# Kernel optimization log

Hardware: AMD Instinct MI355X
Metric: run time of the kernel (lower is better)

Reference implementation:

```python
import jax, jax.numpy as jnp
import numpy as np

B, S, D = 4, 2048, 1024
H, DH = 16, 64
SCALE = DH ** -0.5


def setup_inputs() -> dict:
    key = jax.random.key(0)
    ks = jax.random.split(key, 7)
    x_q = jax.random.normal(ks[0], (B, S, D), dtype=jnp.float32)
    x_k = jax.random.normal(ks[1], (B, S, D), dtype=jnp.float32)
    x_v = jax.random.normal(ks[2], (B, S, D), dtype=jnp.float32)
    # causal mask: True means masked (matches torch masked_fill semantics)
    mask = jnp.triu(jnp.ones((S, S), dtype=bool), k=1)
    # Linear init: randn(in, out) / sqrt(out), no bias
    Wq = jax.random.normal(ks[3], (D, H * DH), dtype=jnp.float32) / np.sqrt(H * DH)
    Wk = jax.random.normal(ks[4], (D, H * DH), dtype=jnp.float32) / np.sqrt(H * DH)
    Wv = jax.random.normal(ks[5], (D, H * DH), dtype=jnp.float32) / np.sqrt(H * DH)
    Wo = jax.random.normal(ks[6], (H * DH, D), dtype=jnp.float32) / np.sqrt(D)
    return {"x_q": x_q, "x_k": x_k, "x_v": x_v, "mask": mask,
            "Wq": Wq, "Wk": Wk, "Wv": Wv, "Wo": Wo}


def reference(x_q, x_k, x_v, mask, Wq, Wk, Wv, Wo):
    def split_heads(x):  # [B,S,H*DH] -> [B,H,S,DH]
        return x.reshape(B, S, H, DH).transpose(0, 2, 1, 3)

    q = split_heads(x_q @ Wq)
    k = split_heads(x_k @ Wk)
    v = split_heads(x_v @ Wv)
    attn = jnp.einsum('bhqd,bhkd->bhqk', q, k) * SCALE
    attn = jnp.where(mask, -jnp.inf, attn)
    w_attn = jax.nn.softmax(attn, axis=-1)  # dropout p=0.0 is identity
    out = jnp.einsum('bhqk,bhkd->bhqd', w_attn, v)
    out = out.transpose(0, 2, 1, 3).reshape(B, S, H * DH)
    return out @ Wo
```

## Files before the change

kernel.cpp:

```cpp
#include <hip/hip_runtime.h>
#include <hip/hip_bf16.h>
#include <math.h>

#define BB 4
#define SS 2048
#define DD 1024
#define HH 16
#define DHE 64
#define NH (HH*DHE)
constexpr float NEG_BIG = -1e30f;

typedef __bf16 bf16x8 __attribute__((ext_vector_type(8)));
typedef float  f32x4  __attribute__((ext_vector_type(4)));

#define WAITVM6()   asm volatile("s_waitcnt vmcnt(6)" ::: "memory")
#define WAITVM4()   asm volatile("s_waitcnt vmcnt(4)" ::: "memory")
#define WAITVM0()   asm volatile("s_waitcnt vmcnt(0)" ::: "memory")
#define WAITLGKM0() asm volatile("s_waitcnt lgkmcnt(0)" ::: "memory")
#define MEMFENCE()  asm volatile("" ::: "memory")

__device__ __forceinline__ void gl_lds16(const __bf16* g, __bf16* l) {
  __builtin_amdgcn_global_load_lds(
      (const __attribute__((address_space(1))) unsigned int*)g,
      (__attribute__((address_space(3))) unsigned int*)l, 16, 0, 0);
}

__device__ __forceinline__ unsigned pack_bf2(float lo, float hi) {
  union { __bf16 h[2]; unsigned u; } p;
  p.h[0] = (__bf16)lo; p.h[1] = (__bf16)hi;
  return p.u;
}

__global__ __launch_bounds__(256) void cvt_k(
    const float* __restrict__ x0, const float* __restrict__ x1,
    const float* __restrict__ x2,
    __bf16* __restrict__ o0, __bf16* __restrict__ o1, __bf16* __restrict__ o2) {
  const float* x = blockIdx.z == 0 ? x0 : blockIdx.z == 1 ? x1 : x2;
  __bf16*      o = blockIdx.z == 0 ? o0 : blockIdx.z == 1 ? o1 : o2;
  const size_t n8 = (size_t)BB * SS * DD / 8;
  for (size_t i = (size_t)blockIdx.x * 256 + threadIdx.x; i < n8;
       i += (size_t)gridDim.x * 256) {
    f32x4 a = *(const f32x4*)(x + i * 8);
    f32x4 b = *(const f32x4*)(x + i * 8 + 4);
    bf16x8 v;
    #pragma unroll
    for (int j = 0; j < 4; j++) { v[j] = (__bf16)a[j]; v[j + 4] = (__bf16)b[j]; }
    *(bf16x8*)(o + i * 8) = v;
  }
}

__global__ __launch_bounds__(256) void wtrans_k(
    const float* __restrict__ w0, const float* __restrict__ w1,
    const float* __restrict__ w2, const float* __restrict__ w3,
    __bf16* __restrict__ o0, __bf16* __restrict__ o1,
    __bf16* __restrict__ o2, __bf16* __restrict__ o3) {
  __shared__ __bf16 t[32][33];
  const float* w = blockIdx.z == 0 ? w0 : blockIdx.z == 1 ? w1 : blockIdx.z == 2 ? w2 : w3;
  __bf16*      o = blockIdx.z == 0 ? o0 : blockIdx.z == 1 ? o1 : blockIdx.z == 2 ? o2 : o3;
  int tx = threadIdx.x & 31, ty = threadIdx.x >> 5;
  int bk = blockIdx.x * 32, bn = blockIdx.y * 32;
  #pragma unroll
  for (int i = 0; i < 4; i++)
    t[ty + i * 8][tx] = (__bf16)w[(size_t)(bk + ty + i * 8) * DD + bn + tx];
  __syncthreads();
  #pragma unroll
  for (int i = 0; i < 4; i++)
    o[(size_t)(bn + ty + i * 8) * DD + bk + tx] = t[tx][ty + i * 8];
}

__global__ __launch_bounds__(256) void vtrans_k(
    const __bf16* __restrict__ v, __bf16* __restrict__ o) {
  __shared__ __bf16 t[32][33];
  int tx = threadIdx.x & 31, ty = threadIdx.x >> 5;
  int bs = blockIdx.x * 32, bc = blockIdx.y * 32;
  const __bf16* vz = v + (size_t)blockIdx.z * SS * NH;
  __bf16*       oz = o + (size_t)blockIdx.z * NH * SS;
  #pragma unroll
  for (int i = 0; i < 4; i++)
    t[ty + i * 8][tx] = vz[(size_t)(bs + ty + i * 8) * NH + bc + tx];
  __syncthreads();
  #pragma unroll
  for (int i = 0; i < 4; i++)
    oz[(size_t)(bc + ty + i * 8) * SS + bs + tx] = t[tx][ty + i * 8];
}

struct B3 {
  const void*  a0; const void*  a1; const void*  a2;
  const __bf16* b0; const __bf16* b1; const __bf16* b2;
  void* c0; void* c1; void* c2;
};

template <typename CT>
__global__ __launch_bounds__(256, 3) void gemm_bb(B3 p) {
  __shared__ __bf16 Asr[3][128][32];
  __shared__ __bf16 Bsr[3][128][32];

  const unsigned nwg  = gridDim.x * gridDim.y * gridDim.z;
  const unsigned flat = blockIdx.x + gridDim.x * (blockIdx.y + gridDim.y * blockIdx.z);
  const unsigned swz  = (flat & 7) * (nwg >> 3) + (flat >> 3);
  const int bx = swz % gridDim.x;
  const unsigned rem = swz / gridDim.x;
  const int by = rem % gridDim.y;
  const int z  = rem / gridDim.y;

  const __bf16* __restrict__ A  = (const __bf16*)(z == 0 ? p.a0 : z == 1 ? p.a1 : p.a2);
  const __bf16* __restrict__ BT = z == 0 ? p.b0 : z == 1 ? p.b1 : p.b2;
  CT* __restrict__ C = (CT*)(z == 0 ? p.c0 : z == 1 ? p.c1 : p.c2);

  const int tid  = threadIdx.x;
  const int wave = tid >> 6, lane = tid & 63;
  const int quad = lane >> 4, l16 = lane & 15;
  const int wr = (wave >> 1) * 64, wc = (wave & 1) * 64;
  const int m0 = by * 128, n0 = bx * 128;

  f32x4 acc[4][4] = {};

  auto issue = [&](int it, int slot) {
    const int k0 = it * 32;
    const int rr  = lane >> 2;
    const int seg = (lane & 3) ^ ((rr >> 1) & 3);
    #pragma unroll
    for (int i = 0; i < 2; i++) {
      const int row = wave * 16 + i * 64 + rr;
      gl_lds16(&A [(size_t)(m0 + row) * DD + k0 + seg * 8], &Asr[slot][wave * 16 + i * 64][0]);
      gl_lds16(&BT[(size_t)(n0 + row) * DD + k0 + seg * 8], &Bsr[slot][wave * 16 + i * 64][0]);
    }
  };

  auto compute = [&](int s) {
    bf16x8 af[4], bfr[4];
    const int ph = (quad ^ ((l16 >> 1) & 3)) * 8;
    #pragma unroll
    for (int t = 0; t < 4; t++) {
      af[t]  = *(const bf16x8*)&Asr[s][wr + t * 16 + l16][ph];
      bfr[t] = *(const bf16x8*)&Bsr[s][wc + t * 16 + l16][ph];
    }
    __builtin_amdgcn_s_setprio(1);
    #pragma unroll
    for (int mt = 0; mt < 4; mt++)
      #pragma unroll
      for (int nt = 0; nt < 4; nt++)
        acc[mt][nt] = __builtin_amdgcn_mfma_f32_16x16x32_bf16(af[mt], bfr[nt], acc[mt][nt], 0, 0, 0);
    __builtin_amdgcn_s_setprio(0);
  };

  issue(0, 0); MEMFENCE();
  issue(1, 1); MEMFENCE();

  int cur = 0, pre = 2;
  #pragma unroll 1
  for (int it = 0; it < 30; it++) {
    WAITVM4();
    __builtin_amdgcn_s_barrier();
    issue(it + 2, pre);
    compute(cur);
    cur = cur == 2 ? 0 : cur + 1;
    pre = pre == 2 ? 0 : pre + 1;
  }
  WAITVM4(); __builtin_amdgcn_s_barrier(); compute(cur);
  cur = cur == 2 ? 0 : cur + 1;
  WAITVM0(); __builtin_amdgcn_s_barrier(); compute(cur);

  #pragma unroll
  for (int mt = 0; mt < 4; mt++)
    #pragma unroll
    for (int nt = 0; nt < 4; nt++)
      #pragma unroll
      for (int r = 0; r < 4; r++) {
        int row = m0 + wr + mt * 16 + quad * 4 + r;
        int col = n0 + wc + nt * 16 + l16;
        C[(size_t)row * NH + col] = (CT)acc[mt][nt][r];
      }
}

template <typename AT> struct AStage;
template <> struct AStage<float>  { f32x4 d[2][2]; };
template <> struct AStage<__bf16> { bf16x8 d[2]; };

template <typename AT, typename CT>
__global__ __launch_bounds__(256, 3) void gemm_bt(B3 p, size_t aoff) {
  __shared__ __bf16 As[128][40];
  __shared__ __bf16 Bs[4][128][32];
  const unsigned nwg  = gridDim.x * gridDim.y * gridDim.z;
  const unsigned flat = blockIdx.x + gridDim.x * (blockIdx.y + gridDim.y * blockIdx.z);
  const unsigned swz  = (flat & 7) * (nwg >> 3) + (flat >> 3);
  const int bx = swz % gridDim.x;
  const unsigned rem = swz / gridDim.x;
  const int by = rem % gridDim.y;
  const int z  = rem / gridDim.y;

  const AT* __restrict__ A = (const AT*)(z == 0 ? p.a0 : z == 1 ? p.a1 : p.a2);
  const __bf16* __restrict__ BT = z == 0 ? p.b0 : z == 1 ? p.b1 : p.b2;
  CT* __restrict__ C = (CT*)(z == 0 ? p.c0 : z == 1 ? p.c1 : p.c2);

  const int tid  = threadIdx.x;
  const int wave = tid >> 6, lane = tid & 63;
  const int quad = lane >> 4, l16 = lane & 15;
  const int wr = (wave >> 1) * 64, wc = (wave & 1) * 64;
  const int m0 = by * 128, n0 = bx * 128;

  f32x4 acc[4][4] = {};
  AStage<AT> aA, aB;

  auto loadA = [&](int k0, AStage<AT>& S) {
    #pragma unroll
    for (int i = 0; i < 2; i++) {
      int c = tid + i * 256;
      int row = c >> 2, seg = (c & 3) * 8;
      if constexpr (sizeof(AT) == 4) {
        const float* ap = (const float*)A + aoff + (size_t)(m0 + row) * DD + k0 + seg;
        S.d[i][0] = *(const f32x4*)ap;
        S.d[i][1] = *(const f32x4*)(ap + 4);
      } else {
        S.d[i] = *(const bf16x8*)((const __bf16*)A + aoff + (size_t)(m0 + row) * DD + k0 + seg);
      }
    }
  };
  auto issueB = [&](int k0, int buf) {
    #pragma unroll
    for (int i = 0; i < 2; i++) {
      int rr  = lane >> 2;
      int row = wave * 16 + i * 64 + rr;
      int seg = (lane & 3) ^ ((rr >> 1) & 3);
      gl_lds16(&BT[(size_t)(n0 + row) * DD + k0 + seg * 8],
               &Bs[buf][wave * 16 + i * 64][0]);
    }
  };

  auto step = [&](int it, AStage<AT>& S, bool last, bool tail) {
    if (last) { WAITVM0(); }
    else if constexpr (sizeof(AT) == 4) { WAITVM6(); }
    else { WAITVM4(); }
    __builtin_amdgcn_s_barrier();
    #pragma unroll
    for (int i = 0; i < 2; i++) {
      int c = tid + i * 256;
      bf16x8 av;
      if constexpr (sizeof(AT) == 4) {
        #pragma unroll
        for (int j = 0; j < 4; j++) {
          av[j]     = (__bf16)S.d[i][0][j];
          av[j + 4] = (__bf16)S.d[i][1][j];
        }
      } else {
        av = S.d[i];
      }
      *(bf16x8*)&As[c >> 2][(c & 3) * 8] = av;
    }
    WAITLGKM0();
    __builtin_amdgcn_s_barrier();
    if (!tail) {
      issueB((it + 2) * 32, (it + 2) & 3);
      loadA((it + 2) * 32, S);
    }
    const int buf = it & 3;
    bf16x8 af[4], bfr[4];
    #pragma unroll
    for (int t = 0; t < 4; t++) {
      af[t]  = *(const bf16x8*)&As[wr + t * 16 + l16][quad * 8];
      bfr[t] = *(const bf16x8*)&Bs[buf][wc + t * 16 + l16][(quad ^ ((l16 >> 1) & 3)) * 8];
    }
    __builtin_amdgcn_s_setprio(1);
    #pragma unroll
    for (int mt = 0; mt < 4; mt++)
      #pragma unroll
      for (int nt = 0; nt < 4; nt++)
        acc[mt][nt] = __builtin_amdgcn_mfma_f32_16x16x32_bf16(af[mt], bfr[nt], acc[mt][nt], 0, 0, 0);
    __builtin_amdgcn_s_setprio(0);
  };

  issueB(0, 0);  loadA(0, aA);
  MEMFENCE();
  issueB(32, 1); loadA(32, aB);
  MEMFENCE();

  for (int it2 = 0; it2 < 15; it2++) {
    step(2 * it2,     aA, false, false);
    step(2 * it2 + 1, aB, false, false);
  }
  step(30, aA, false, true);
  step(31, aB, true,  true);

  #pragma unroll
  for (int mt = 0; mt < 4; mt++)
    #pragma unroll
    for (int nt = 0; nt < 4; nt++)
      #pragma unroll
      for (int r = 0; r < 4; r++) {
        int row = m0 + wr + mt * 16 + quad * 4 + r;
        int col = n0 + wc + nt * 16 + l16;
        C[(size_t)row * NH + col] = (CT)acc[mt][nt][r];
      }
}

__global__ __launch_bounds__(256, 4) void attn_k(
    const __bf16* __restrict__ Q, const __bf16* __restrict__ K,
    const __bf16* __restrict__ VT, __bf16* __restrict__ O) {
  __shared__ __bf16 Ks[64][68];
  __shared__ __bf16 Vs[64][68];

  const int tid  = threadIdx.x;
  const int wave = tid >> 6, lane = tid & 63;
  const int quad = lane >> 4, l16 = lane & 15;

  const int n    = blockIdx.x;
  const int xcd  = n & 7, slot = n >> 3;
  const int gidx = xcd + 8 * (slot >> 4);
  const int bx   = slot & 15;
  const int h = gidx & 15, z = gidx >> 4;

  const __bf16* Qg = Q + (size_t)z * SS * NH + h * DHE;
  const __bf16* Kg = K + (size_t)z * SS * NH + h * DHE;
  const __bf16* Vg = VT + ((size_t)z * HH + h) * DHE * SS;
  __bf16*       Og = O + (size_t)z * SS * NH + h * DHE;

  bf16x8 kreg[2], vreg[2];
  auto loadKV = [&](int k0) {
    #pragma unroll
    for (int i = 0; i < 2; i++) {
      int v = tid + i * 256;
      kreg[i] = *(const bf16x8*)&Kg[(size_t)(k0 + (v >> 3)) * NH + (v & 7) * 8];
      vreg[i] = *(const bf16x8*)&Vg[(size_t)(v >> 3) * SS + k0 + (v & 7) * 8];
    }
  };

  #pragma unroll 1
  for (int seg = 0; seg < 2; seg++) {
    const int qt = seg ? bx : 31 - bx;
    const int q0 = qt * 64;
    const int ntiles = qt + 1;

    const int qrow = q0 + wave * 16 + l16;
    bf16x8 qf[2];
    #pragma unroll
    for (int kk = 0; kk < 2; kk++) {
      bf16x8 t = *(const bf16x8*)&Qg[(size_t)qrow * NH + kk * 32 + quad * 8];
      #pragma unroll
      for (int j = 0; j < 8; j++) t[j] = (__bf16)((float)t[j] * 0.125f);
      qf[kk] = t;
    }

    loadKV(0);
    float prows = 0.f;
    f32x4 oacc[4] = {};

    for (int kt = 0; kt < ntiles; kt++) {
      const int k0 = kt * 64;
      __syncthreads();
      #pragma unroll
      for (int i = 0; i < 2; i++) {
        int v = tid + i * 256;
        *(bf16x8*)&Ks[v >> 3][(v & 7) * 8] = kreg[i];
        *(bf16x8*)&Vs[v >> 3][(v & 7) * 8] = vreg[i];
      }
      __syncthreads();
      if (kt + 1 < ntiles) loadKV(k0 + 64);

      const bool diag = (kt == ntiles - 1);
      const int nq  = diag ? wave + 1 : 4;
      const int nsm = diag ? ((wave + 2) & ~1) : 4;
      const int nkk = nsm >> 1;

      f32x4 sc[4] = {};
      __builtin_amdgcn_s_setprio(1);
      #pragma unroll
      for (int kk = 0; kk < 2; kk++)
        #pragma unroll
        for (int nt = 0; nt < 4; nt++)
          if (nt < nq) {
            bf16x8 kf = *(const bf16x8*)&Ks[nt * 16 + l16][kk * 32 + quad * 8];
            sc[nt] = __builtin_amdgcn_mfma_f32_16x16x32_bf16(kf, qf[kk], sc[nt], 0, 0, 0);
          }
      __builtin_amdgcn_s_setprio(0);

      bf16x8 pf[2];
      #pragma unroll
      for (int t = 0; t < 2; t++)
        if (t < nkk) {
          const int nt0 = 2 * t, nt1 = 2 * t + 1;
          float pA[4], pB[4];
          #pragma unroll
          for (int r = 0; r < 4; r++) {
            float v0 = sc[nt0][r], v1 = sc[nt1][r];
            if (diag) {
              const int kb = k0 + quad * 4 + r;
              if (kb + nt0 * 16 > qrow) v0 = NEG_BIG;
              if (kb + nt1 * 16 > qrow) v1 = NEG_BIG;
            }
            pA[r] = __expf(v0); pB[r] = __expf(v1);
            prows += pA[r] + pB[r];
          }
          unsigned a0 = pack_bf2(pA[0], pA[1]), a1 = pack_bf2(pA[2], pA[3]);
          unsigned b0 = pack_bf2(pB[0], pB[1]), b1 = pack_bf2(pB[2], pB[3]);
          unsigned x0 = (quad & 1) ? a0 : b0, x1 = (quad & 1) ? a1 : b1;
          unsigned y0 = (quad & 1) ? b0 : a0, y1 = (quad & 1) ? b1 : a1;
          unsigned r16_0 = __shfl_xor((int)x0, 16), r16_1 = __shfl_xor((int)x1, 16);
          unsigned r32_0 = __shfl_xor((int)x0, 32), r32_1 = __shfl_xor((int)x1, 32);
          unsigned r48_0 = __shfl_xor((int)y0, 48), r48_1 = __shfl_xor((int)y1, 48);
          unsigned w0 = quad == 0 ? a0    : quad == 1 ? r48_0 : quad == 2 ? r32_0 : r16_0;
          unsigned w1 = quad == 0 ? a1    : quad == 1 ? r48_1 : quad == 2 ? r32_1 : r16_1;
          unsigned w2 = quad == 0 ? r16_0 : quad == 1 ? r32_0 : quad == 2 ? r48_0 : b0;
          unsigned w3 = quad == 0 ? r16_1 : quad == 1 ? r32_1 : quad == 2 ? r48_1 : b1;
          union { unsigned u[4]; bf16x8 v; } asm_;
          asm_.u[0] = w0; asm_.u[1] = w1; asm_.u[2] = w2; asm_.u[3] = w3;
          pf[t] = asm_.v;
        }

      __builtin_amdgcn_s_setprio(1);
      #pragma unroll
      for (int kk = 0; kk < 2; kk++)
        if (kk < nkk) {
          #pragma unroll
          for (int dt = 0; dt < 4; dt++) {
            bf16x8 vf = *(const bf16x8*)&Vs[dt * 16 + l16][kk * 32 + quad * 8];
            oacc[dt] = __builtin_amdgcn_mfma_f32_16x16x32_bf16(pf[kk], vf, oacc[dt], 0, 0, 0);
          }
        }
      __builtin_amdgcn_s_setprio(0);
    }

    prows += __shfl_xor(prows, 16, 64);
    prows += __shfl_xor(prows, 32, 64);

    #pragma unroll
    for (int r = 0; r < 4; r++) {
      float tot = __shfl(prows, quad * 4 + r, 64);
      float inv = tot > 0.f ? 1.0f / tot : 0.f;
      int qg = q0 + wave * 16 + quad * 4 + r;
      #pragma unroll
      for (int dt = 0; dt < 4; dt++)
        Og[(size_t)qg * NH + dt * 16 + l16] = (__bf16)(oacc[dt][r] * inv);
    }
  }
}

extern "C" void kernel_launch(void* const* d_in, const int* in_sizes, int n_in,
                              void* d_out, int out_size, void* d_ws, size_t ws_size,
                              hipStream_t stream) {
  const float* x_q = (const float*)d_in[0];
  const float* x_k = (const float*)d_in[1];
  const float* x_v = (const float*)d_in[2];
  const float* Wq = (const float*)d_in[4];
  const float* Wk = (const float*)d_in[5];
  const float* Wv = (const float*)d_in[6];
  const float* Wo = (const float*)d_in[7];
  float* out = (float*)d_out;

  const size_t WTE = (size_t)DD * NH;
  const size_t PB  = (size_t)SS * NH;
  const size_t FULLB = (size_t)BB * PB;

  char* ws = (char*)d_ws;
  __bf16* WqT = (__bf16*)ws;
  __bf16* WkT = WqT + WTE;
  __bf16* WvT = WkT + WTE;
  __bf16* WoT = WvT + WTE;
  __bf16* buf0 = WoT + WTE;

  wtrans_k<<<dim3(32, 32, 4), 256, 0, stream>>>(Wq, Wk, Wv, Wo, WqT, WkT, WvT, WoT);

  const size_t needFast = 4 * WTE * 2 + 4 * FULLB * 2 + 3 * FULLB * 2;
  const size_t needFull = 4 * WTE * 2 + 4 * FULLB * 2;
  if (ws_size >= needFast) {
    __bf16* Qb  = buf0;
    __bf16* Kb  = Qb + FULLB;
    __bf16* Vb  = Kb + FULLB;
    __bf16* VT  = Vb + FULLB;
    __bf16* xqb = VT + FULLB;
    __bf16* xkb = xqb + FULLB;
    __bf16* xvb = xkb + FULLB;
    __bf16* Ob  = Vb;
    cvt_k<<<dim3(1024, 1, 3), 256, 0, stream>>>(x_q, x_k, x_v, xqb, xkb, xvb);
    B3 qkv = { xqb, xkb, xvb, WqT, WkT, WvT, Qb, Kb, Vb };
    gemm_bb<__bf16><<<dim3(8, 64, 3), 256, 0, stream>>>(qkv);
    vtrans_k<<<dim3(SS / 32, NH / 32, BB), 256, 0, stream>>>(Vb, VT);
    attn_k<<<dim3((SS / 128) * HH * BB), 256, 0, stream>>>(Qb, Kb, VT, Ob);
    B3 og = { Ob, Ob, Ob, WoT, WoT, WoT, out, out, out };
    gemm_bb<float><<<dim3(8, 64, 1), 256, 0, stream>>>(og);
  } else if (ws_size >= needFull) {
    __bf16* Qb = buf0;
    __bf16* Kb = Qb + FULLB;
    __bf16* Vb = Kb + FULLB;
    __bf16* VT = Vb + FULLB;
    __bf16* Ob = Vb;
    B3 qkv = { x_q, x_k, x_v, WqT, WkT, WvT, Qb, Kb, Vb };
    gemm_bt<float, __bf16><<<dim3(8, 64, 3), 256, 0, stream>>>(qkv, 0);
    vtrans_k<<<dim3(SS / 32, NH / 32, BB), 256, 0, stream>>>(Vb, VT);
    attn_k<<<dim3((SS / 128) * HH * BB), 256, 0, stream>>>(Qb, Kb, VT, Ob);
    B3 og = { Ob, Ob, Ob, WoT, WoT, WoT, out, out, out };
    gemm_bt<__bf16, float><<<dim3(8, 64, 1), 256, 0, stream>>>(og, 0);
  } else {
    __bf16* Qb = buf0;
    __bf16* Kb = Qb + PB;
    __bf16* Vb = Kb + PB;
    __bf16* VT = Vb + PB;
    __bf16* Ob = Vb;
    for (int b = 0; b < BB; b++) {
      const size_t boff = (size_t)b * PB;
      B3 qkv = { x_q, x_k, x_v, WqT, WkT, WvT, Qb, Kb, Vb };
      gemm_bt<float, __bf16><<<dim3(8, 16, 3), 256, 0, stream>>>(qkv, boff);
      vtrans_k<<<dim3(SS / 32, NH / 32, 1), 256, 0, stream>>>(Vb, VT);
      attn_k<<<dim3((SS / 128) * HH), 256, 0, stream>>>(Qb, Kb, VT, Ob);
      B3 og = { Ob, Ob, Ob, WoT, WoT, WoT, out + boff, out + boff, out + boff };
      gemm_bt<__bf16, float><<<dim3(8, 16, 1), 256, 0, stream>>>(og, 0);
    }
  }
}
```

Baseline: 334.2 us.

## Fuse V transpose into QKV GEMM epilogue, fold softmax scale into Wk, shrink attention blocks

The QKV GEMM now writes the V projection directly in transposed layout through an LDS staging tile, which removes the separate vtrans_k launch and its extra global round-trip. The softmax scale times log2(e) is folded into Wk during weight conversion, so attention skips the per-element Q scaling and uses the hardware exp2 instead of __expf. The attention kernel moves to 128-thread blocks covering 32 query rows, which doubles the number of blocks and adjusts the causal diagonal handling for odd half-tiles. Rounding the scaled Wk to bf16 changes numerics slightly, and the smaller blocks load each K/V tile for half as many query rows.

```diff
diff --git a/kernel.cpp b/kernel.cpp
--- a/kernel.cpp
+++ b/kernel.cpp
@@ -9,6 +9,7 @@
 #define DHE 64
 #define NH (HH*DHE)
 constexpr float NEG_BIG = -1e30f;
+constexpr float K_PRESCALE = 0.18033688f;
 
 typedef __bf16 bf16x8 __attribute__((ext_vector_type(8)));
 typedef float  f32x4  __attribute__((ext_vector_type(4)));
@@ -57,11 +58,12 @@
   __shared__ __bf16 t[32][33];
   const float* w = blockIdx.z == 0 ? w0 : blockIdx.z == 1 ? w1 : blockIdx.z == 2 ? w2 : w3;
   __bf16*      o = blockIdx.z == 0 ? o0 : blockIdx.z == 1 ? o1 : blockIdx.z == 2 ? o2 : o3;
+  const float sc = blockIdx.z == 1 ? K_PRESCALE : 1.0f;
   int tx = threadIdx.x & 31, ty = threadIdx.x >> 5;
   int bk = blockIdx.x * 32, bn = blockIdx.y * 32;
   #pragma unroll
   for (int i = 0; i < 4; i++)
-    t[ty + i * 8][tx] = (__bf16)w[(size_t)(bk + ty + i * 8) * DD + bn + tx];
+    t[ty + i * 8][tx] = (__bf16)(w[(size_t)(bk + ty + i * 8) * DD + bn + tx] * sc);
   __syncthreads();
   #pragma unroll
   for (int i = 0; i < 4; i++)
@@ -91,9 +93,11 @@
 };
 
 template <typename CT>
-__global__ __launch_bounds__(256, 3) void gemm_bb(B3 p) {
-  __shared__ __bf16 Asr[3][128][32];
-  __shared__ __bf16 Bsr[3][128][32];
+__global__ __launch_bounds__(256, 3) void gemm_bb(B3 p, int vz) {
+  __shared__ __align__(16) __bf16 smbuf[24576];
+  __bf16 (*Asr)[128][32] = (__bf16 (*)[128][32])smbuf;
+  __bf16 (*Bsr)[128][32] = (__bf16 (*)[128][32])(smbuf + 12288);
+  __bf16 (*smT)[136]     = (__bf16 (*)[136])smbuf;
 
   const unsigned nwg  = gridDim.x * gridDim.y * gridDim.z;
   const unsigned flat = blockIdx.x + gridDim.x * (blockIdx.y + gridDim.y * blockIdx.z);
@@ -161,6 +165,31 @@
   cur = cur == 2 ? 0 : cur + 1;
   WAITVM0(); __builtin_amdgcn_s_barrier(); compute(cur);
 
+  if constexpr (sizeof(CT) == 2) {
+    if (z == vz) {
+      __syncthreads();
+      #pragma unroll
+      for (int mt = 0; mt < 4; mt++)
+        #pragma unroll
+        for (int nt = 0; nt < 4; nt++)
+          #pragma unroll
+          for (int r = 0; r < 4; r++)
+            smT[wc + nt * 16 + l16][wr + mt * 16 + quad * 4 + r] = (__bf16)acc[mt][nt][r];
+      __syncthreads();
+      const int b  = m0 >> 11;
+      const int s0 = m0 & 2047;
+      __bf16* VTp = (__bf16*)C + (size_t)b * NH * SS;
+      const int sseg = (tid & 15) * 8;
+      #pragma unroll
+      for (int g = 0; g < 8; g++) {
+        const int cl = (tid >> 4) + g * 16;
+        bf16x8 vv = *(const bf16x8*)&smT[cl][sseg];
+        *(bf16x8*)&VTp[(size_t)(n0 + cl) * SS + s0 + sseg] = vv;
+      }
+      return;
+    }
+  }
+
   #pragma unroll
   for (int mt = 0; mt < 4; mt++)
     #pragma unroll
@@ -293,7 +322,7 @@
       }
 }
 
-__global__ __launch_bounds__(256, 4) void attn_k(
+__global__ __launch_bounds__(128, 4) void attn_k(
     const __bf16* __restrict__ Q, const __bf16* __restrict__ K,
     const __bf16* __restrict__ VT, __bf16* __restrict__ O) {
   __shared__ __bf16 Ks[64][68];
@@ -305,8 +334,8 @@
 
   const int n    = blockIdx.x;
   const int xcd  = n & 7, slot = n >> 3;
-  const int gidx = xcd + 8 * (slot >> 4);
-  const int bx   = slot & 15;
+  const int gidx = xcd + 8 * (slot >> 5);
+  const int bx   = slot & 31;
   const int h = gidx & 15, z = gidx >> 4;
 
   const __bf16* Qg = Q + (size_t)z * SS * NH + h * DHE;
@@ -314,11 +343,11 @@
   const __bf16* Vg = VT + ((size_t)z * HH + h) * DHE * SS;
   __bf16*       Og = O + (size_t)z * SS * NH + h * DHE;
 
-  bf16x8 kreg[2], vreg[2];
+  bf16x8 kreg[4], vreg[4];
   auto loadKV = [&](int k0) {
     #pragma unroll
-    for (int i = 0; i < 2; i++) {
-      int v = tid + i * 256;
+    for (int i = 0; i < 4; i++) {
+      int v = tid + i * 128;
       kreg[i] = *(const bf16x8*)&Kg[(size_t)(k0 + (v >> 3)) * NH + (v & 7) * 8];
       vreg[i] = *(const bf16x8*)&Vg[(size_t)(v >> 3) * SS + k0 + (v & 7) * 8];
     }
@@ -326,19 +355,16 @@
 
   #pragma unroll 1
   for (int seg = 0; seg < 2; seg++) {
-    const int qt = seg ? bx : 31 - bx;
-    const int q0 = qt * 64;
-    const int ntiles = qt + 1;
+    const int qt2 = seg ? bx : 63 - bx;
+    const int q0 = qt2 * 32;
+    const int ntiles = qt2 / 2 + 1;
+    const int qpar = qt2 & 1;
 
     const int qrow = q0 + wave * 16 + l16;
     bf16x8 qf[2];
     #pragma unroll
-    for (int kk = 0; kk < 2; kk++) {
-      bf16x8 t = *(const bf16x8*)&Qg[(size_t)qrow * NH + kk * 32 + quad * 8];
-      #pragma unroll
-      for (int j = 0; j < 8; j++) t[j] = (__bf16)((float)t[j] * 0.125f);
-      qf[kk] = t;
-    }
+    for (int kk = 0; kk < 2; kk++)
+      qf[kk] = *(const bf16x8*)&Qg[(size_t)qrow * NH + kk * 32 + quad * 8];
 
     loadKV(0);
     float prows = 0.f;
@@ -348,8 +374,8 @@
       const int k0 = kt * 64;
       __syncthreads();
       #pragma unroll
-      for (int i = 0; i < 2; i++) {
-        int v = tid + i * 256;
+      for (int i = 0; i < 4; i++) {
+        int v = tid + i * 128;
         *(bf16x8*)&Ks[v >> 3][(v & 7) * 8] = kreg[i];
         *(bf16x8*)&Vs[v >> 3][(v & 7) * 8] = vreg[i];
       }
@@ -357,8 +383,8 @@
       if (kt + 1 < ntiles) loadKV(k0 + 64);
 
       const bool diag = (kt == ntiles - 1);
-      const int nq  = diag ? wave + 1 : 4;
-      const int nsm = diag ? ((wave + 2) & ~1) : 4;
+      const int nq  = diag ? (qpar ? wave + 3 : wave + 1) : 4;
+      const int nsm = (nq + 1) & ~1;
       const int nkk = nsm >> 1;
 
       f32x4 sc[4] = {};
@@ -387,7 +413,8 @@
               if (kb + nt0 * 16 > qrow) v0 = NEG_BIG;
               if (kb + nt1 * 16 > qrow) v1 = NEG_BIG;
             }
-            pA[r] = __expf(v0); pB[r] = __expf(v1);
+            pA[r] = __builtin_amdgcn_exp2f(v0);
+            pB[r] = __builtin_amdgcn_exp2f(v1);
             prows += pA[r] + pB[r];
           }
           unsigned a0 = pack_bf2(pA[0], pA[1]), a1 = pack_bf2(pA[2], pA[3]);
@@ -471,12 +498,11 @@
     __bf16* xvb = xkb + FULLB;
     __bf16* Ob  = Vb;
     cvt_k<<<dim3(1024, 1, 3), 256, 0, stream>>>(x_q, x_k, x_v, xqb, xkb, xvb);
-    B3 qkv = { xqb, xkb, xvb, WqT, WkT, WvT, Qb, Kb, Vb };
-    gemm_bb<__bf16><<<dim3(8, 64, 3), 256, 0, stream>>>(qkv);
-    vtrans_k<<<dim3(SS / 32, NH / 32, BB), 256, 0, stream>>>(Vb, VT);
-    attn_k<<<dim3((SS / 128) * HH * BB), 256, 0, stream>>>(Qb, Kb, VT, Ob);
+    B3 qkv = { xqb, xkb, xvb, WqT, WkT, WvT, Qb, Kb, VT };
+    gemm_bb<__bf16><<<dim3(8, 64, 3), 256, 0, stream>>>(qkv, 2);
+    attn_k<<<dim3((SS / 64) * HH * BB), 128, 0, stream>>>(Qb, Kb, VT, Ob);
     B3 og = { Ob, Ob, Ob, WoT, WoT, WoT, out, out, out };
-    gemm_bb<float><<<dim3(8, 64, 1), 256, 0, stream>>>(og);
+    gemm_bb<float><<<dim3(8, 64, 1), 256, 0, stream>>>(og, -1);
   } else if (ws_size >= needFull) {
     __bf16* Qb = buf0;
     __bf16* Kb = Qb + FULLB;
@@ -486,7 +512,7 @@
     B3 qkv = { x_q, x_k, x_v, WqT, WkT, WvT, Qb, Kb, Vb };
     gemm_bt<float, __bf16><<<dim3(8, 64, 3), 256, 0, stream>>>(qkv, 0);
     vtrans_k<<<dim3(SS / 32, NH / 32, BB), 256, 0, stream>>>(Vb, VT);
-    attn_k<<<dim3((SS / 128) * HH * BB), 256, 0, stream>>>(Qb, Kb, VT, Ob);
+    attn_k<<<dim3((SS / 64) * HH * BB), 128, 0, stream>>>(Qb, Kb, VT, Ob);
     B3 og = { Ob, Ob, Ob, WoT, WoT, WoT, out, out, out };
     gemm_bt<__bf16, float><<<dim3(8, 64, 1), 256, 0, stream>>>(og, 0);
   } else {
@@ -500,7 +526,7 @@
       B3 qkv = { x_q, x_k, x_v, WqT, WkT, WvT, Qb, Kb, Vb };
       gemm_bt<float, __bf16><<<dim3(8, 16, 3), 256, 0, stream>>>(qkv, boff);
       vtrans_k<<<dim3(SS / 32, NH / 32, 1), 256, 0, stream>>>(Vb, VT);
-      attn_k<<<dim3((SS / 128) * HH), 256, 0, stream>>>(Qb, Kb, VT, Ob);
+      attn_k<<<dim3((SS / 64) * HH), 128, 0, stream>>>(Qb, Kb, VT, Ob);
       B3 og = { Ob, Ob, Ob, WoT, WoT, WoT, out + boff, out + boff, out + boff };
       gemm_bt<__bf16, float><<<dim3(8, 16, 1), 256, 0, stream>>>(og, 0);
     }
```

New measurement: 349.9 us. 4.7% more time.
